# Optimization experiments

Measured on AMD Instinct MI355X. Metric: run time of the kernel, lower is better.

Reference implementation:

```python
import jax, jax.numpy as jnp
import numpy as np

C = 256
CQK = C // 8  # 32

def setup_inputs() -> dict:
    key = jax.random.key(0)
    ks = jax.random.split(key, 9)
    B, H, W = 4, 64, 64
    shp = (B, C, H, W)
    v = jax.random.normal(ks[0], shp, dtype=jnp.float32)
    k = jax.random.normal(ks[1], shp, dtype=jnp.float32)
    q = jax.random.normal(ks[2], shp, dtype=jnp.float32)
    s = 1.0 / np.sqrt(C)
    Wq = jax.random.normal(ks[3], (CQK, C), dtype=jnp.float32) * s
    bq = jnp.zeros((CQK,), dtype=jnp.float32)
    Wk = jax.random.normal(ks[4], (CQK, C), dtype=jnp.float32) * s
    bk = jnp.zeros((CQK,), dtype=jnp.float32)
    Wv = jax.random.normal(ks[5], (C, C), dtype=jnp.float32) * s
    bv = jnp.zeros((C,), dtype=jnp.float32)
    # torch inits gamma=0 (out == v); use small nonzero so attention path is exercised
    gamma = jnp.full((1,), 0.5, dtype=jnp.float32)
    return {"v": v, "k": k, "q": q, "Wq": Wq, "bq": bq, "Wk": Wk, "bk": bk,
            "Wv": Wv, "bv": bv, "gamma": gamma}

def reference(v, k, q, Wq, bq, Wk, bk, Wv, bv, gamma):
    B, Cc, Hh, Ww = v.shape
    N = Hh * Ww
    # 1x1 convs == per-pixel channel matmuls
    pq = jnp.einsum('oc,bchw->bohw', Wq, q) + bq[None, :, None, None]  # B,CQK,H,W
    pk = jnp.einsum('oc,bchw->bohw', Wk, k) + bk[None, :, None, None]
    pv = jnp.einsum('oc,bchw->bohw', Wv, v) + bv[None, :, None, None]  # B,C,H,W
    pq = pq.reshape(B, -1, N)  # B,d,N
    pk = pk.reshape(B, -1, N)
    pv = pv.reshape(B, Cc, N)
    # energy[b,n,m] = <q_n, k_m>; softmax over m (keys)
    energy = jnp.einsum('bdn,bdm->bnm', pq, pk)
    attn = jax.nn.softmax(energy, axis=-1)
    # out[b,c,n] = sum_m v[b,c,m] * attn[b,n,m]
    out = jnp.einsum('bcm,bnm->bcn', pv, attn).reshape(B, Cc, Hh, Ww)
    return gamma * out + v
```

## Files before the change

kernel.cpp:

```cpp
#include <hip/hip_runtime.h>
#include <hip/hip_bf16.h>

typedef __attribute__((ext_vector_type(8))) short short8_t;
typedef __attribute__((ext_vector_type(4))) short short4_t;
typedef __attribute__((ext_vector_type(4))) float float4_t;

#define B_   4
#define C_   256
#define N_   4096
#define DQK  32
#define LOG2E 1.4426950408889634f

#define VMCNT12  asm volatile("s_waitcnt vmcnt(12)" ::: "memory")
#define VMCNT4   asm volatile("s_waitcnt vmcnt(4)" ::: "memory")
#define LGKM0    asm volatile("s_waitcnt lgkmcnt(0)" ::: "memory")
#define SBAR     __builtin_amdgcn_s_barrier()
#define SCHEDB   __builtin_amdgcn_sched_barrier(0)

__device__ __forceinline__ unsigned short f2bf(float x) {
    union { float f; unsigned int u; } v; v.f = x;
    unsigned int r = v.u + 0x7FFFu + ((v.u >> 16) & 1u);
    return (unsigned short)(r >> 16);
}
__device__ __forceinline__ unsigned short f2bf_hw(float x) {
    return __bfloat16_as_ushort(__float2bfloat16(x));
}

__global__ __launch_bounds__(256) void cast_w_k(
        const float* __restrict__ Wq, const float* __restrict__ Wk,
        const float* __restrict__ Wv,
        unsigned short* __restrict__ Wqb, unsigned short* __restrict__ Wkb,
        unsigned short* __restrict__ Wvb) {
    int i = blockIdx.x * 256 + threadIdx.x;
    if (i < 8192)            Wqb[i] = f2bf(Wq[i]);
    else if (i < 16384)      Wkb[i - 8192] = f2bf(Wk[i - 8192]);
    else                     Wvb[i - 16384] = f2bf(Wv[i - 16384]);
}

__global__ __launch_bounds__(256) void proj_qk_k(
        const float* __restrict__ q_in, const float* __restrict__ k_in,
        const unsigned short* __restrict__ Wqb, const unsigned short* __restrict__ Wkb,
        const float* __restrict__ bq, const float* __restrict__ bk,
        unsigned short* __restrict__ pqT, unsigned short* __restrict__ pkT) {
    int b = blockIdx.y, z = blockIdx.z;
    const float* X = z ? k_in : q_in;
    const unsigned short* W = z ? Wkb : Wqb;
    const float* bias = z ? bk : bq;
    unsigned short* P = z ? pkT : pqT;
    float scl = z ? 1.0f : LOG2E;
    int tid = threadIdx.x, wave = tid >> 6, lane = tid & 63, l15 = lane & 15, g = lane >> 4;
    int nb = blockIdx.x * 64 + wave * 16;
    float4_t acc0 = {0.f, 0.f, 0.f, 0.f}, acc1 = {0.f, 0.f, 0.f, 0.f};
    const float* Xcol = X + (size_t)b * C_ * N_ + nb + l15;
#pragma unroll
    for (int kk = 0; kk < 8; ++kk) {
        short8_t a;
#pragma unroll
        for (int j = 0; j < 8; ++j)
            a[j] = (short)f2bf(Xcol[(size_t)(kk * 32 + 8 * g + j) * N_]);
        short8_t b0 = *(const short8_t*)(W + (size_t)l15 * C_ + kk * 32 + 8 * g);
        short8_t b1 = *(const short8_t*)(W + (size_t)(16 + l15) * C_ + kk * 32 + 8 * g);
        acc0 = __builtin_amdgcn_mfma_f32_16x16x32_bf16(a, b0, acc0, 0, 0, 0);
        acc1 = __builtin_amdgcn_mfma_f32_16x16x32_bf16(a, b1, acc1, 0, 0, 0);
    }
#pragma unroll
    for (int r = 0; r < 4; ++r) {
        int n = nb + 4 * g + r;
        P[((size_t)b * N_ + n) * DQK + l15]      = f2bf((acc0[r] + bias[l15]) * scl);
        P[((size_t)b * N_ + n) * DQK + 16 + l15] = f2bf((acc1[r] + bias[16 + l15]) * scl);
    }
}

__global__ __launch_bounds__(256) void proj_v_k(
        const float* __restrict__ v_in, const unsigned short* __restrict__ Wvb,
        const float* __restrict__ bv, unsigned short* __restrict__ pv) {
    int b = blockIdx.y;
    int tid = threadIdx.x, wave = tid >> 6, lane = tid & 63, l15 = lane & 15, g = lane >> 4;
    int mb = blockIdx.x * 16;
    int m = mb + l15;
    int k32 = m & 31;
    int pcol = (k32 < 16) ? ((k32 >> 2) * 8 + (k32 & 3))
                          : (((k32 - 16) >> 2) * 8 + 4 + (k32 & 3));
    int mcol = (m & ~31) + pcol;
    float4_t acc[4];
#pragma unroll
    for (int i = 0; i < 4; ++i) acc[i] = (float4_t){0.f, 0.f, 0.f, 0.f};
    const float* Vcol = v_in + (size_t)b * C_ * N_ + mb + l15;
#pragma unroll
    for (int kk = 0; kk < 8; ++kk) {
        short8_t bf;
#pragma unroll
        for (int j = 0; j < 8; ++j)
            bf[j] = (short)f2bf(Vcol[(size_t)(kk * 32 + 8 * g + j) * N_]);
#pragma unroll
        for (int ct = 0; ct < 4; ++ct) {
            short8_t af = *(const short8_t*)(Wvb + (size_t)(wave * 64 + ct * 16 + l15) * C_ + kk * 32 + 8 * g);
            acc[ct] = __builtin_amdgcn_mfma_f32_16x16x32_bf16(af, bf, acc[ct], 0, 0, 0);
        }
    }
#pragma unroll
    for (int ct = 0; ct < 4; ++ct)
#pragma unroll
        for (int r = 0; r < 4; ++r) {
            int c = wave * 64 + ct * 16 + 4 * g + r;
            pv[((size_t)b * C_ + c) * N_ + mcol] = f2bf(acc[ct][r] + bv[c]);
        }
}

__global__ __launch_bounds__(256, 2) void attn_split_k(
        const unsigned short* __restrict__ pqT, const unsigned short* __restrict__ pkT,
        const unsigned short* __restrict__ pv,
        float* __restrict__ accP, float* __restrict__ lP, int KS) {
    __shared__ __align__(16) unsigned short VT[2][256][64];
    __shared__ __align__(16) short8_t Pl[2][4][2][4][16];
    int nqb = gridDim.x;
    int lin = blockIdx.x + nqb * (blockIdx.y + KS * blockIdx.z);
    int cpx = (nqb * KS * 4) >> 3;
    int sl  = (lin & 7) * cpx + (lin >> 3);
    int qbi = sl % nqb;
    int s   = (sl / nqb) % KS;
    int b   = sl / (nqb * KS);

    int kps = N_ / KS, ks0 = s * kps, nt = kps >> 6;
    int tid = threadIdx.x, wave = tid >> 6, lane = tid & 63, l15 = lane & 15, g = lane >> 4;
    int qb = qbi * 64;
    int sw = (l15 & 7) << 4;
    int rl = lane >> 3, cl = (lane & 7) ^ rl;

    short8_t qf = *(const short8_t*)(pqT + ((size_t)b * N_ + qb + wave * 16 + l15) * DQK + 8 * g);
    float4_t acc[4][4];
#pragma unroll
    for (int i = 0; i < 4; ++i)
#pragma unroll
        for (int j = 0; j < 4; ++j) acc[i][j] = (float4_t){0.f, 0.f, 0.f, 0.f};
    float4_t accl = {0.f, 0.f, 0.f, 0.f};
    short8_t onef;
#pragma unroll
    for (int j = 0; j < 8; ++j) onef[j] = (short)0x3F80;
    const float4_t zero4 = {0.f, 0.f, 0.f, 0.f};
    const char* pvb8 = (const char*)(pv + (size_t)b * C_ * N_);
    const char* pkTb = (const char*)pkT + (size_t)b * N_ * DQK * 2;

    unsigned soff[8];
#pragma unroll
    for (int i = 0; i < 8; ++i)
        soff[i] = (unsigned)(((wave * 64 + i * 8 + rl) * N_ + ks0 + 8 * cl) * 2);
    unsigned koff = (unsigned)(((ks0 + l15) * DQK + 8 * g) * 2);
    const char* vbA = (const char*)&VT[0][0][0] + (wave * 64 + l15) * 128 + ((16 * g) ^ sw);
    const char* vbB = (const char*)&VT[0][0][0] + (wave * 64 + l15) * 128 + ((64 + 16 * g) ^ sw);

#define STAGE(RBUF)                                                           \
    _Pragma("unroll")                                                         \
    for (int i_ = 0; i_ < 8; ++i_) {                                          \
        __builtin_amdgcn_global_load_lds(                                     \
            (const __attribute__((address_space(1))) unsigned int*)(const void*)(pvb8 + soff[i_]), \
            (__attribute__((address_space(3))) unsigned int*)(void*)&VT[RBUF][wave * 64 + i_ * 8][0], 16, 0, 0); \
        soff[i_] += 128;                                                      \
    }

#define KFLOAD(DST)                                                           \
    _Pragma("unroll")                                                         \
    for (int it_ = 0; it_ < 4; ++it_)                                         \
        DST[it_] = *(const short8_t*)(pkTb + koff + it_ * 1024);              \
    koff += 4096;

#define VREAD(DST, RB)                                                        \
    _Pragma("unroll")                                                         \
    for (int ct_ = 0; ct_ < 4; ++ct_) {                                       \
        DST[ct_][0] = *(const short8_t*)(vbA + (RB) * 32768 + ct_ * 2048);    \
        DST[ct_][1] = *(const short8_t*)(vbB + (RB) * 32768 + ct_ * 2048);    \
    }

#define PFREAD(DST, CB)                                                       \
    _Pragma("unroll")                                                         \
    for (int qt_ = 0; qt_ < 4; ++qt_)                                         \
        _Pragma("unroll")                                                     \
        for (int kh_ = 0; kh_ < 2; ++kh_)                                     \
            DST[qt_][kh_] = Pl[CB][qt_][kh_][g][l15];

#define QKWR(KF, NB)                                                          \
    {                                                                          \
        float4_t sv_[4];                                                       \
        _Pragma("unroll")                                                      \
        for (int it_ = 0; it_ < 4; ++it_)                                      \
            sv_[it_] = __builtin_amdgcn_mfma_f32_16x16x32_bf16(KF[it_], qf, zero4, 0, 0, 0); \
        float p_[16];                                                          \
        _Pragma("unroll")                                                      \
        for (int it_ = 0; it_ < 4; ++it_)                                      \
            _Pragma("unroll")                                                  \
            for (int r_ = 0; r_ < 4; ++r_)                                     \
                p_[it_ * 4 + r_] = exp2f(sv_[it_][r_]);                        \
        short8_t pbn0_, pbn1_;                                                 \
        _Pragma("unroll")                                                      \
        for (int j_ = 0; j_ < 4; ++j_) {                                       \
            pbn0_[j_]     = (short)f2bf_hw(p_[j_]);                            \
            pbn0_[4 + j_] = (short)f2bf_hw(p_[4 + j_]);                        \
            pbn1_[j_]     = (short)f2bf_hw(p_[8 + j_]);                        \
            pbn1_[4 + j_] = (short)f2bf_hw(p_[12 + j_]);                       \
        }                                                                      \
        accl = __builtin_amdgcn_mfma_f32_16x16x32_bf16(onef, pbn0_, accl, 0, 0, 0); \
        accl = __builtin_amdgcn_mfma_f32_16x16x32_bf16(onef, pbn1_, accl, 0, 0, 0); \
        Pl[NB][wave][0][g][l15] = pbn0_;                                       \
        Pl[NB][wave][1][g][l15] = pbn1_;                                       \
    }

#define PVM_ALL(VF, PF)                                                       \
    _Pragma("unroll")                                                         \
    for (int ct_ = 0; ct_ < 4; ++ct_)                                         \
        _Pragma("unroll")                                                     \
        for (int qt_ = 0; qt_ < 4; ++qt_) {                                   \
            acc[ct_][qt_] = __builtin_amdgcn_mfma_f32_16x16x32_bf16(VF[ct_][0], PF[qt_][0], acc[ct_][qt_], 0, 0, 0); \
            acc[ct_][qt_] = __builtin_amdgcn_mfma_f32_16x16x32_bf16(VF[ct_][1], PF[qt_][1], acc[ct_][qt_], 0, 0, 0); \
        }

#define BODY(T, RB, KFC, CB, NB)                                              \
    {                                                                          \
        if ((T) + 1 < nt) { STAGE((RB) ^ 1) VMCNT12; } else { VMCNT4; }        \
        SCHEDB;                                                                \
        short8_t vf_[4][2], pf_[4][2];                                         \
        VREAD(vf_, RB)                                                         \
        PFREAD(pf_, CB)                                                        \
        if ((T) + 1 < nt) { QKWR(KFC, NB) }                                    \
        KFLOAD(KFC)                                                            \
        __builtin_amdgcn_s_setprio(1);                                         \
        PVM_ALL(vf_, pf_)                                                      \
        __builtin_amdgcn_s_setprio(0);                                         \
        LGKM0; SCHEDB;                                                         \
        SBAR;                                                                  \
    }

    short8_t kfA[4], kfB[4];
    STAGE(0)
    KFLOAD(kfA)
    KFLOAD(kfB)
    QKWR(kfA, 0)
    KFLOAD(kfA)
    LGKM0; SCHEDB;
    SBAR;

    for (int t = 0; t < nt; t += 2) {
        BODY(t,     0, kfB, 0, 1)
        BODY(t + 1, 1, kfA, 1, 0)
    }

    if (g == 0)
        lP[(size_t)(b * KS + s) * N_ + qb + wave * 16 + l15] = accl[0];
    float* accOut = accP + ((size_t)(b * KS + s) * C_) * N_;
#pragma unroll
    for (int ct = 0; ct < 4; ++ct)
#pragma unroll
        for (int qt = 0; qt < 4; ++qt)
#pragma unroll
            for (int r = 0; r < 4; ++r) {
                int c = wave * 64 + ct * 16 + 4 * g + r;
                accOut[(size_t)c * N_ + qb + qt * 16 + l15] = acc[ct][qt][r];
            }
#undef STAGE
#undef KFLOAD
#undef VREAD
#undef PFREAD
#undef QKWR
#undef PVM_ALL
#undef BODY
}

__global__ __launch_bounds__(256) void combine_k(
        const float* __restrict__ accP, const float* __restrict__ lP,
        const float* __restrict__ v_in, const float* __restrict__ gamma,
        float* __restrict__ out, int KS) {
    int i = blockIdx.x * 256 + threadIdx.x;
    const int nq4 = N_ / 4;
    int q0 = (i % nq4) * 4;
    int c  = (i / nq4) % C_;
    int b  = i / (nq4 * C_);
    float4_t num = {0.f, 0.f, 0.f, 0.f}, den = {0.f, 0.f, 0.f, 0.f};
    for (int s = 0; s < KS; ++s) {
        float4_t l4 = *(const float4_t*)(lP + (size_t)(b * KS + s) * N_ + q0);
        float4_t a4 = *(const float4_t*)(accP + ((size_t)(b * KS + s) * C_ + c) * N_ + q0);
#pragma unroll
        for (int j = 0; j < 4; ++j) {
            den[j] += l4[j];
            num[j] += a4[j];
        }
    }
    float gm = gamma[0];
    size_t idx = ((size_t)(b * C_ + c)) * N_ + q0;
    float4_t vi = *(const float4_t*)(v_in + idx);
    float4_t o;
#pragma unroll
    for (int j = 0; j < 4; ++j) o[j] = gm * num[j] / den[j] + vi[j];
    *(float4_t*)(out + idx) = o;
}

extern "C" void kernel_launch(void* const* d_in, const int* in_sizes, int n_in,
                              void* d_out, int out_size, void* d_ws, size_t ws_size,
                              hipStream_t stream) {
    (void)in_sizes; (void)n_in; (void)out_size;
    const float* v_in  = (const float*)d_in[0];
    const float* k_in  = (const float*)d_in[1];
    const float* q_in  = (const float*)d_in[2];
    const float* Wq    = (const float*)d_in[3];
    const float* bq    = (const float*)d_in[4];
    const float* Wk    = (const float*)d_in[5];
    const float* bk    = (const float*)d_in[6];
    const float* Wv    = (const float*)d_in[7];
    const float* bv    = (const float*)d_in[8];
    const float* gamma = (const float*)d_in[9];
    float* out = (float*)d_out;

    char* ws = (char*)d_ws;
    unsigned short* pvb = (unsigned short*)(ws + 0);
    unsigned short* pqT = (unsigned short*)(ws + 8388608);
    unsigned short* pkT = (unsigned short*)(ws + 9437184);
    unsigned short* Wqb = (unsigned short*)(ws + 10502144);
    unsigned short* Wkb = (unsigned short*)(ws + 10518528);
    unsigned short* Wvb = (unsigned short*)(ws + 10534912);
    const size_t base2 = 10665984;

    int KS = 2;
    while (KS > 1) {
        size_t need = base2 + (size_t)KS * 16777216 + (size_t)KS * 262144;
        if (need <= ws_size) break;
        KS >>= 1;
    }
    float* accP = (float*)(ws + base2);
    float* lP   = (float*)(ws + base2 + (size_t)KS * 16777216);

    cast_w_k<<<320, 256, 0, stream>>>(Wq, Wk, Wv, Wqb, Wkb, Wvb);
    proj_qk_k<<<dim3(64, 4, 2), 256, 0, stream>>>(q_in, k_in, Wqb, Wkb, bq, bk, pqT, pkT);
    proj_v_k<<<dim3(256, 4), 256, 0, stream>>>(v_in, Wvb, bv, pvb);
    attn_split_k<<<dim3(64, KS, 4), 256, 0, stream>>>(pqT, pkT, pvb, accP, lP, KS);
    combine_k<<<4096, 256, 0, stream>>>(accP, lP, v_in, gamma, out, KS);
}
```

Baseline: 99.76 us.

## Single-buffer V tile, bf16 partial accumulators, raise occupancy and split-K to four

The attention kernel drops the double-buffered V LDS tile for a single buffer and reorders the loop body so the next V stage and K fragment loads are issued after the LDS reads. This halves LDS use so launch bounds can allow three blocks per CU. Partial output accumulators are written as bf16 instead of fp32, which halves combine traffic and lets the split-K factor go from two to four for more parallelism. The cost is less latency hiding from the single buffer, extra rounding error in the partial sums, and more partials to combine.

```diff
diff --git a/kernel.cpp b/kernel.cpp
--- a/kernel.cpp
+++ b/kernel.cpp
@@ -3,6 +3,7 @@
 
 typedef __attribute__((ext_vector_type(8))) short short8_t;
 typedef __attribute__((ext_vector_type(4))) short short4_t;
+typedef __attribute__((ext_vector_type(4))) unsigned short ushort4_t;
 typedef __attribute__((ext_vector_type(4))) float float4_t;
 
 #define B_   4
@@ -11,7 +12,6 @@
 #define DQK  32
 #define LOG2E 1.4426950408889634f
 
-#define VMCNT12  asm volatile("s_waitcnt vmcnt(12)" ::: "memory")
 #define VMCNT4   asm volatile("s_waitcnt vmcnt(4)" ::: "memory")
 #define LGKM0    asm volatile("s_waitcnt lgkmcnt(0)" ::: "memory")
 #define SBAR     __builtin_amdgcn_s_barrier()
@@ -24,6 +24,9 @@
 }
 __device__ __forceinline__ unsigned short f2bf_hw(float x) {
     return __bfloat16_as_ushort(__float2bfloat16(x));
+}
+__device__ __forceinline__ float bf2f(unsigned short u) {
+    union { unsigned int u; float f; } v; v.u = ((unsigned int)u) << 16; return v.f;
 }
 
 __global__ __launch_bounds__(256) void cast_w_k(
@@ -107,11 +110,11 @@
         }
 }
 
-__global__ __launch_bounds__(256, 2) void attn_split_k(
+__global__ __launch_bounds__(256, 3) void attn_split_k(
         const unsigned short* __restrict__ pqT, const unsigned short* __restrict__ pkT,
         const unsigned short* __restrict__ pv,
-        float* __restrict__ accP, float* __restrict__ lP, int KS) {
-    __shared__ __align__(16) unsigned short VT[2][256][64];
+        unsigned short* __restrict__ accP, float* __restrict__ lP, int KS) {
+    __shared__ __align__(16) unsigned short VT[256][64];
     __shared__ __align__(16) short8_t Pl[2][4][2][4][16];
     int nqb = gridDim.x;
     int lin = blockIdx.x + nqb * (blockIdx.y + KS * blockIdx.z);
@@ -146,15 +149,15 @@
     for (int i = 0; i < 8; ++i)
         soff[i] = (unsigned)(((wave * 64 + i * 8 + rl) * N_ + ks0 + 8 * cl) * 2);
     unsigned koff = (unsigned)(((ks0 + l15) * DQK + 8 * g) * 2);
-    const char* vbA = (const char*)&VT[0][0][0] + (wave * 64 + l15) * 128 + ((16 * g) ^ sw);
-    const char* vbB = (const char*)&VT[0][0][0] + (wave * 64 + l15) * 128 + ((64 + 16 * g) ^ sw);
-
-#define STAGE(RBUF)                                                           \
+    const char* vbA = (const char*)&VT[0][0] + (wave * 64 + l15) * 128 + ((16 * g) ^ sw);
+    const char* vbB = (const char*)&VT[0][0] + (wave * 64 + l15) * 128 + ((64 + 16 * g) ^ sw);
+
+#define STAGE()                                                               \
     _Pragma("unroll")                                                         \
     for (int i_ = 0; i_ < 8; ++i_) {                                          \
         __builtin_amdgcn_global_load_lds(                                     \
             (const __attribute__((address_space(1))) unsigned int*)(const void*)(pvb8 + soff[i_]), \
-            (__attribute__((address_space(3))) unsigned int*)(void*)&VT[RBUF][wave * 64 + i_ * 8][0], 16, 0, 0); \
+            (__attribute__((address_space(3))) unsigned int*)(void*)&VT[wave * 64 + i_ * 8][0], 16, 0, 0); \
         soff[i_] += 128;                                                      \
     }
 
@@ -164,11 +167,11 @@
         DST[it_] = *(const short8_t*)(pkTb + koff + it_ * 1024);              \
     koff += 4096;
 
-#define VREAD(DST, RB)                                                        \
+#define VREAD(DST)                                                            \
     _Pragma("unroll")                                                         \
     for (int ct_ = 0; ct_ < 4; ++ct_) {                                       \
-        DST[ct_][0] = *(const short8_t*)(vbA + (RB) * 32768 + ct_ * 2048);    \
-        DST[ct_][1] = *(const short8_t*)(vbB + (RB) * 32768 + ct_ * 2048);    \
+        DST[ct_][0] = *(const short8_t*)(vbA + ct_ * 2048);                   \
+        DST[ct_][1] = *(const short8_t*)(vbB + ct_ * 2048);                   \
     }
 
 #define PFREAD(DST, CB)                                                       \
@@ -213,39 +216,38 @@
             acc[ct_][qt_] = __builtin_amdgcn_mfma_f32_16x16x32_bf16(VF[ct_][1], PF[qt_][1], acc[ct_][qt_], 0, 0, 0); \
         }
 
-#define BODY(T, RB, KFC, CB, NB)                                              \
+#define BODY(T, KFC, KFN, CB, NB)                                             \
     {                                                                          \
-        if ((T) + 1 < nt) { STAGE((RB) ^ 1) VMCNT12; } else { VMCNT4; }        \
-        SCHEDB;                                                                \
+        VMCNT4; SCHEDB;                                                        \
         short8_t vf_[4][2], pf_[4][2];                                         \
-        VREAD(vf_, RB)                                                         \
+        VREAD(vf_)                                                             \
         PFREAD(pf_, CB)                                                        \
-        if ((T) + 1 < nt) { QKWR(KFC, NB) }                                    \
-        KFLOAD(KFC)                                                            \
+        LGKM0; SCHEDB;                                                         \
+        if ((T) + 1 < nt) { STAGE() KFLOAD(KFN) }                              \
         __builtin_amdgcn_s_setprio(1);                                         \
         PVM_ALL(vf_, pf_)                                                      \
         __builtin_amdgcn_s_setprio(0);                                         \
+        if ((T) + 1 < nt) { QKWR(KFC, NB) }                                    \
         LGKM0; SCHEDB;                                                         \
         SBAR;                                                                  \
     }
 
     short8_t kfA[4], kfB[4];
-    STAGE(0)
+    STAGE()
     KFLOAD(kfA)
     KFLOAD(kfB)
     QKWR(kfA, 0)
-    KFLOAD(kfA)
     LGKM0; SCHEDB;
     SBAR;
 
     for (int t = 0; t < nt; t += 2) {
-        BODY(t,     0, kfB, 0, 1)
-        BODY(t + 1, 1, kfA, 1, 0)
+        BODY(t,     kfB, kfA, 0, 1)
+        BODY(t + 1, kfA, kfB, 1, 0)
     }
 
     if (g == 0)
         lP[(size_t)(b * KS + s) * N_ + qb + wave * 16 + l15] = accl[0];
-    float* accOut = accP + ((size_t)(b * KS + s) * C_) * N_;
+    unsigned short* accOut = accP + ((size_t)(b * KS + s) * C_) * N_;
 #pragma unroll
     for (int ct = 0; ct < 4; ++ct)
 #pragma unroll
@@ -253,7 +255,7 @@
 #pragma unroll
             for (int r = 0; r < 4; ++r) {
                 int c = wave * 64 + ct * 16 + 4 * g + r;
-                accOut[(size_t)c * N_ + qb + qt * 16 + l15] = acc[ct][qt][r];
+                accOut[(size_t)c * N_ + qb + qt * 16 + l15] = f2bf_hw(acc[ct][qt][r]);
             }
 #undef STAGE
 #undef KFLOAD
@@ -265,7 +267,7 @@
 }
 
 __global__ __launch_bounds__(256) void combine_k(
-        const float* __restrict__ accP, const float* __restrict__ lP,
+        const unsigned short* __restrict__ accP, const float* __restrict__ lP,
         const float* __restrict__ v_in, const float* __restrict__ gamma,
         float* __restrict__ out, int KS) {
     int i = blockIdx.x * 256 + threadIdx.x;
@@ -276,11 +278,11 @@
     float4_t num = {0.f, 0.f, 0.f, 0.f}, den = {0.f, 0.f, 0.f, 0.f};
     for (int s = 0; s < KS; ++s) {
         float4_t l4 = *(const float4_t*)(lP + (size_t)(b * KS + s) * N_ + q0);
-        float4_t a4 = *(const float4_t*)(accP + ((size_t)(b * KS + s) * C_ + c) * N_ + q0);
+        ushort4_t a4 = *(const ushort4_t*)(accP + ((size_t)(b * KS + s) * C_ + c) * N_ + q0);
 #pragma unroll
         for (int j = 0; j < 4; ++j) {
             den[j] += l4[j];
-            num[j] += a4[j];
+            num[j] += bf2f(a4[j]);
         }
     }
     float gm = gamma[0];
@@ -317,14 +319,14 @@
     unsigned short* Wvb = (unsigned short*)(ws + 10534912);
     const size_t base2 = 10665984;
 
-    int KS = 2;
+    int KS = 4;
     while (KS > 1) {
-        size_t need = base2 + (size_t)KS * 16777216 + (size_t)KS * 262144;
+        size_t need = base2 + (size_t)KS * 8388608 + (size_t)KS * 65536;
         if (need <= ws_size) break;
         KS >>= 1;
     }
-    float* accP = (float*)(ws + base2);
-    float* lP   = (float*)(ws + base2 + (size_t)KS * 16777216);
+    unsigned short* accP = (unsigned short*)(ws + base2);
+    float* lP = (float*)(ws + base2 + (size_t)KS * 8388608);
 
     cast_w_k<<<320, 256, 0, stream>>>(Wq, Wk, Wv, Wqb, Wkb, Wvb);
     proj_qk_k<<<dim3(64, 4, 2), 256, 0, stream>>>(q_in, k_in, Wqb, Wkb, bq, bk, pqT, pkT);
```

New measurement: 140.0 us. 1.4x slower.
